# Optimization experiments

Measured on AMD Instinct MI355X. Metric: run time of the kernel, lower is better.

Reference implementation:

```python
import jax, jax.numpy as jnp
import numpy as np


def setup_inputs() -> dict:
    key = jax.random.key(0)
    k1, k2 = jax.random.split(key)
    imgs = jax.random.normal(k1, (4, 16, 64, 64), dtype=jnp.float32)
    kernel = jax.random.normal(k2, (16, 16, 5, 5), dtype=jnp.float32)
    return {"imgs": imgs, "kernel": kernel, "stride": 1, "padding": 2}


def reference(imgs, kernel, stride, padding):
    # Tropical-max (T+) semifield convolution (morphological dilation):
    #   multiply = add, add_reduce = max, zero = -inf, kind='conv' (kernel flipped)
    B, C, H, W = imgs.shape
    O, _, kH, kW = kernel.shape
    x = jnp.pad(imgs, ((0, 0), (0, 0), (padding, padding), (padding, padding)),
                constant_values=-jnp.inf)
    # kind='conv' flips the kernel spatially
    k = kernel[:, :, ::-1, ::-1]
    # im2col-style window extraction: [B, C*kH*kW, oH, oW], channel-major (C, kH, kW)
    patches = jax.lax.conv_general_dilated_patches(
        x, (kH, kW), (stride, stride), padding="VALID")
    oH, oW = patches.shape[2], patches.shape[3]
    win = patches.reshape(B, 1, C, kH, kW, oH, oW)
    w = k.reshape(1, O, C, kH, kW, 1, 1)
    # broadcast semifield multiply (add), then semifield reduce (max) over (C, kH, kW)
    out = jnp.max(win + w, axis=(2, 3, 4))  # [B, O, oH, oW]
    return out
```

## Files before the change

kernel.cpp:

```cpp
#include <hip/hip_runtime.h>
#include <math.h>


#define NEG_INF (-__builtin_inff())
#define PW 68
#define PPLANE (PW * PW)

typedef float f32x2  __attribute__((ext_vector_type(2)));
typedef float f32x4u __attribute__((ext_vector_type(4), aligned(4)));

__global__ __launch_bounds__(256) void pad_kernel(
        const float* __restrict__ img, float* __restrict__ pad) {
    const int idx4  = blockIdx.x * 256 + threadIdx.x;
    const int plane = idx4 / 1156;
    const int r4    = idx4 - plane * 1156;
    const int py    = r4 / 17;
    const int px0   = (r4 - py * 17) * 4;
    const int yy    = py - 2;
    const bool yok  = (unsigned)yy < 64u;
    const float* src = img + (plane << 12) + ((yok ? yy : 0) << 6);
    float o[4];
#pragma unroll
    for (int t = 0; t < 4; ++t) {
        int xx = px0 + t - 2;
        bool ok = yok && ((unsigned)xx < 64u);
        o[t] = ok ? src[(unsigned)xx < 64u ? xx : 0] : NEG_INF;
    }
    float4* dst = (float4*)(pad + plane * PPLANE + py * PW + px0);
    *dst = make_float4(o[0], o[1], o[2], o[3]);
}

__global__ __launch_bounds__(512, 8) void bconv_kernel(
        const float* __restrict__ pad,
        const float* __restrict__ kern,
        float* __restrict__ out) {
    const int x  = threadIdx.x & 63;
    const int w  = __builtin_amdgcn_readfirstlane(threadIdx.x >> 6);
    const int y  = blockIdx.x;
    const int og = blockIdx.y;
    const int b  = blockIdx.z;
    const int o0 = og * 4;
    const int c0 = w * 2;

    __shared__ float red[8][4][64];

    float acc0 = NEG_INF, acc1 = NEG_INF, acc2 = NEG_INF, acc3 = NEG_INF;

#pragma unroll 1
    for (int cc = 0; cc < 2; ++cc) {
        const int c = c0 + cc;
        const float* __restrict__ pl = pad + (b * 16 + c) * PPLANE + y * PW + x;

        float v[5][5];
#pragma unroll
        for (int i = 0; i < 5; ++i) {
            f32x4u v4 = *(const f32x4u*)(pl + i * PW);
            v[i][0] = v4.x; v[i][1] = v4.y; v[i][2] = v4.z; v[i][3] = v4.w;
            v[i][4] = pl[i * PW + 4];
        }

#define ACC_O(oo, A)                                                          \
        {                                                                     \
            const float* __restrict__ kp = kern + ((o0 + oo) * 16 + c) * 25;  \
            _Pragma("unroll")                                                 \
            for (int g = 0; g < 5; ++g) {                                     \
                const int kb = 24 - g * 5;                                    \
                f32x2 a01 = (f32x2){v[g][0], v[g][1]}                         \
                          + (f32x2){kp[kb], kp[kb - 1]};                      \
                f32x2 a23 = (f32x2){v[g][2], v[g][3]}                         \
                          + (f32x2){kp[kb - 2], kp[kb - 3]};                  \
                float a4  = v[g][4] + kp[kb - 4];                             \
                float m01 = fmaxf(a01.x, a01.y);                              \
                float m234 = fmaxf(fmaxf(a23.x, a23.y), a4);                  \
                A = fmaxf(A, fmaxf(m01, m234));                               \
            }                                                                 \
        }
        ACC_O(0, acc0)
        ACC_O(1, acc1)
        ACC_O(2, acc2)
        ACC_O(3, acc3)
#undef ACC_O
    }

    red[w][0][x] = acc0;
    red[w][1][x] = acc1;
    red[w][2][x] = acc2;
    red[w][3][x] = acc3;
    __syncthreads();

    if (threadIdx.x < 256) {
        const int oo = threadIdx.x >> 6;
        float r = red[0][oo][x];
#pragma unroll
        for (int ww = 1; ww < 8; ++ww) r = fmaxf(r, red[ww][oo][x]);
        out[((b * 16 + o0 + oo) << 12) + (y << 6) + x] = r;
    }
}

extern "C" void kernel_launch(void* const* d_in, const int* in_sizes, int n_in,
                              void* d_out, int out_size, void* d_ws, size_t ws_size,
                              hipStream_t stream) {
    const float* img  = (const float*)d_in[0];
    const float* kern = (const float*)d_in[1];
    float* out = (float*)d_out;
    float* pad = (float*)d_ws;
    (void)in_sizes; (void)n_in; (void)out_size; (void)ws_size;

    hipLaunchKernelGGL(pad_kernel, dim3(289), dim3(256), 0, stream, img, pad);

    dim3 grid(64, 4, 4);
    hipLaunchKernelGGL(bconv_kernel, grid, dim3(512), 0, stream, pad, kern, out);
}
```

Measured before the change: 66.28 us.

## Fuse padding into conv kernel with LDS staging and eight outputs per block

Removes the separate pad kernel and its global workspace round trip. Each block now stages the five needed input rows for all 16 channels into shared memory, inserting -inf for the padded border. Each block computes 8 output channels instead of 4, so the grid has half as many blocks. The cost is an extra LDS staging phase with integer divides and a barrier, higher register pressure from 8 accumulators (launch bounds drop to 4 blocks per SM), and fewer blocks, 512 in total.

```diff
diff --git a/kernel.cpp b/kernel.cpp
--- a/kernel.cpp
+++ b/kernel.cpp
@@ -3,98 +3,83 @@
 
 
 #define NEG_INF (-__builtin_inff())
-#define PW 68
-#define PPLANE (PW * PW)
+#define ROWW   68
+#define CPLANE (5 * ROWW)
+#define STAGE_N (16 * CPLANE)
 
-typedef float f32x2  __attribute__((ext_vector_type(2)));
-typedef float f32x4u __attribute__((ext_vector_type(4), aligned(4)));
+typedef float f32x2 __attribute__((ext_vector_type(2)));
 
-__global__ __launch_bounds__(256) void pad_kernel(
-        const float* __restrict__ img, float* __restrict__ pad) {
-    const int idx4  = blockIdx.x * 256 + threadIdx.x;
-    const int plane = idx4 / 1156;
-    const int r4    = idx4 - plane * 1156;
-    const int py    = r4 / 17;
-    const int px0   = (r4 - py * 17) * 4;
-    const int yy    = py - 2;
-    const bool yok  = (unsigned)yy < 64u;
-    const float* src = img + (plane << 12) + ((yok ? yy : 0) << 6);
-    float o[4];
-#pragma unroll
-    for (int t = 0; t < 4; ++t) {
-        int xx = px0 + t - 2;
-        bool ok = yok && ((unsigned)xx < 64u);
-        o[t] = ok ? src[(unsigned)xx < 64u ? xx : 0] : NEG_INF;
-    }
-    float4* dst = (float4*)(pad + plane * PPLANE + py * PW + px0);
-    *dst = make_float4(o[0], o[1], o[2], o[3]);
-}
-
-__global__ __launch_bounds__(512, 8) void bconv_kernel(
-        const float* __restrict__ pad,
+__global__ __launch_bounds__(512, 4) void bconv_fused(
+        const float* __restrict__ img,
         const float* __restrict__ kern,
         float* __restrict__ out) {
-    const int x  = threadIdx.x & 63;
-    const int w  = __builtin_amdgcn_readfirstlane(threadIdx.x >> 6);
-    const int y  = blockIdx.x;
-    const int og = blockIdx.y;
-    const int b  = blockIdx.z;
-    const int o0 = og * 4;
-    const int c0 = w * 2;
+    const int tid = threadIdx.x;
+    const int x   = tid & 63;
+    const int w   = __builtin_amdgcn_readfirstlane(tid >> 6);
+    const int y   = blockIdx.x;
+    const int og  = blockIdx.y;
+    const int b   = blockIdx.z;
 
-    __shared__ float red[8][4][64];
+    __shared__ float tap[STAGE_N];
+    __shared__ float red[8][8][64];
 
-    float acc0 = NEG_INF, acc1 = NEG_INF, acc2 = NEG_INF, acc3 = NEG_INF;
+    const float* __restrict__ imgb = img + (b << 14);
+    for (int k = tid; k < STAGE_N; k += 512) {
+        const int c   = k / CPLANE;
+        const int rem = k - c * CPLANE;
+        const int r   = rem / ROWW;
+        const int col = rem - r * ROWW - 2;
+        const int row = y + r - 2;
+        const bool ok = ((unsigned)row < 64u) & ((unsigned)col < 64u);
+        const int idx = ok ? ((c << 12) + (row << 6) + col) : 0;
+        tap[k] = ok ? imgb[idx] : NEG_INF;
+    }
+    __syncthreads();
 
-#pragma unroll 1
+    const int c0     = w * 2;
+    const int o_base = og * 8;
+
+    float acc[8];
+#pragma unroll
+    for (int o = 0; o < 8; ++o) acc[o] = NEG_INF;
+
+#pragma unroll
     for (int cc = 0; cc < 2; ++cc) {
         const int c = c0 + cc;
-        const float* __restrict__ pl = pad + (b * 16 + c) * PPLANE + y * PW + x;
+        const float* tp = &tap[c * CPLANE + x];
 
         float v[5][5];
 #pragma unroll
-        for (int i = 0; i < 5; ++i) {
-            f32x4u v4 = *(const f32x4u*)(pl + i * PW);
-            v[i][0] = v4.x; v[i][1] = v4.y; v[i][2] = v4.z; v[i][3] = v4.w;
-            v[i][4] = pl[i * PW + 4];
+        for (int i = 0; i < 5; ++i)
+#pragma unroll
+            for (int j = 0; j < 5; ++j)
+                v[i][j] = tp[i * ROWW + j];
+
+#pragma unroll
+        for (int o = 0; o < 8; ++o) {
+            const float* __restrict__ kp = kern + ((o_base + o) * 16 + c) * 25;
+#pragma unroll
+            for (int g = 0; g < 5; ++g) {
+                const int kb = 24 - g * 5;
+                f32x2 a01 = (f32x2){v[g][0], v[g][1]} + (f32x2){kp[kb],     kp[kb - 1]};
+                f32x2 a23 = (f32x2){v[g][2], v[g][3]} + (f32x2){kp[kb - 2], kp[kb - 3]};
+                float a4  = v[g][4] + kp[kb - 4];
+                float m01  = fmaxf(a01.x, a01.y);
+                float m234 = fmaxf(fmaxf(a23.x, a23.y), a4);
+                acc[o] = fmaxf(acc[o], fmaxf(m01, m234));
+            }
         }
-
-#define ACC_O(oo, A)                                                          \
-        {                                                                     \
-            const float* __restrict__ kp = kern + ((o0 + oo) * 16 + c) * 25;  \
-            _Pragma("unroll")                                                 \
-            for (int g = 0; g < 5; ++g) {                                     \
-                const int kb = 24 - g * 5;                                    \
-                f32x2 a01 = (f32x2){v[g][0], v[g][1]}                         \
-                          + (f32x2){kp[kb], kp[kb - 1]};                      \
-                f32x2 a23 = (f32x2){v[g][2], v[g][3]}                         \
-                          + (f32x2){kp[kb - 2], kp[kb - 3]};                  \
-                float a4  = v[g][4] + kp[kb - 4];                             \
-                float m01 = fmaxf(a01.x, a01.y);                              \
-                float m234 = fmaxf(fmaxf(a23.x, a23.y), a4);                  \
-                A = fmaxf(A, fmaxf(m01, m234));                               \
-            }                                                                 \
-        }
-        ACC_O(0, acc0)
-        ACC_O(1, acc1)
-        ACC_O(2, acc2)
-        ACC_O(3, acc3)
-#undef ACC_O
     }
 
-    red[w][0][x] = acc0;
-    red[w][1][x] = acc1;
-    red[w][2][x] = acc2;
-    red[w][3][x] = acc3;
+#pragma unroll
+    for (int o = 0; o < 8; ++o) red[w][o][x] = acc[o];
     __syncthreads();
 
-    if (threadIdx.x < 256) {
-        const int oo = threadIdx.x >> 6;
-        float r = red[0][oo][x];
+    const int oo = tid >> 6;
+    float r = red[0][oo][x];
 #pragma unroll
-        for (int ww = 1; ww < 8; ++ww) r = fmaxf(r, red[ww][oo][x]);
-        out[((b * 16 + o0 + oo) << 12) + (y << 6) + x] = r;
-    }
+    for (int ww = 1; ww < 8; ++ww) r = fmaxf(r, red[ww][oo][x]);
+    out[((b * 16 + o_base + oo) << 12) + (y << 6) + x] = r;
 }
 
 extern "C" void kernel_launch(void* const* d_in, const int* in_sizes, int n_in,
@@ -103,11 +88,8 @@
     const float* img  = (const float*)d_in[0];
     const float* kern = (const float*)d_in[1];
     float* out = (float*)d_out;
-    float* pad = (float*)d_ws;
-    (void)in_sizes; (void)n_in; (void)out_size; (void)ws_size;
+    (void)in_sizes; (void)n_in; (void)out_size; (void)d_ws; (void)ws_size;
 
-    hipLaunchKernelGGL(pad_kernel, dim3(289), dim3(256), 0, stream, img, pad);
-
-    dim3 grid(64, 4, 4);
-    hipLaunchKernelGGL(bconv_kernel, grid, dim3(512), 0, stream, pad, kern, out);
+    dim3 grid(64, 2, 4);
+    hipLaunchKernelGGL(bconv_fused, grid, dim3(512), 0, stream, img, kern, out);
 }
```

New measurement: 67.72 us. 1.02x slower.
